# Kernel tuning notes

Hardware: AMD Instinct MI355X
Metric: run time of the kernel (lower is better)

## Reference

```python
import jax, jax.numpy as jnp
import numpy as np

N_NODES = 50000
N_EDGES = 1600000
D_IN = 512
D_OUT = 512


def setup_inputs() -> dict:
    key = jax.random.key(0)
    k1, k2, k3, k4, k5, k6 = jax.random.split(key, 6)
    stdv = 1.0 / np.sqrt(D_OUT)
    x = jax.random.normal(k1, (N_NODES, D_IN), dtype=jnp.float32)
    weight = jax.random.uniform(k2, (D_IN, D_OUT), dtype=jnp.float32, minval=-stdv, maxval=stdv)
    bias = jax.random.uniform(k3, (1, D_OUT), dtype=jnp.float32, minval=-stdv, maxval=stdv)
    edge_val = jax.random.uniform(k4, (N_EDGES,), dtype=jnp.float32)
    edge_row = jax.random.randint(k5, (N_EDGES,), 0, N_NODES, dtype=jnp.int64)
    edge_col = jax.random.randint(k6, (N_EDGES,), 0, N_NODES, dtype=jnp.int64)
    return {"x": x, "weight": weight, "bias": bias,
            "edge_val": edge_val, "edge_row": edge_row, "edge_col": edge_col}


def reference(x, weight, bias, edge_val, edge_row, edge_col):
    # hidden = X @ W  : [N, D_OUT] dense GEMM
    hidden = jnp.matmul(x, weight)
    # spmm: out[i] = sum over edges (i <- j) of adj_val * hidden[j]
    msgs = edge_val[:, None] * hidden[edge_col]            # [E, D_OUT]
    out = jax.ops.segment_sum(msgs, edge_row, num_segments=N_NODES)
    return out + bias
```

## Files before the change

### kernel.cpp

```cpp
#include <hip/hip_runtime.h>

typedef short short8 __attribute__((ext_vector_type(8)));
typedef float v4f   __attribute__((ext_vector_type(4)));

#define N_NODES 50000
#define N_EDGES 1600000
#define DIM     512
#define SCAN_NB 49

__device__ __forceinline__ float bf2f(unsigned short u) {
    unsigned int x = ((unsigned int)u) << 16;
    return __uint_as_float(x);
}
__device__ __forceinline__ unsigned int f2bfu(float f) {
    unsigned int x = __float_as_uint(f);
    unsigned int r = x + 0x7fffu + ((x >> 16) & 1u);
    return r >> 16;
}

__global__ void detect_kernel(const unsigned int* __restrict__ xw,
                              const int* __restrict__ erow,
                              int* __restrict__ flags) {
    __shared__ int cbf, cz;
    if (threadIdx.x == 0) { cbf = 0; cz = 0; }
    __syncthreads();
    int lb = 0, lz = 0;
    for (int i = threadIdx.x; i < 1024; i += 256) {
        unsigned int w = xw[i];
        unsigned int e0 = (w >> 7) & 0xFFu;
        unsigned int e1 = (w >> 23) & 0xFFu;
        if (e0 >= 0x70u && e0 <= 0x8Fu && e1 >= 0x70u && e1 <= 0x8Fu) lb++;
        if (erow[2 * i + 1] == 0) lz++;
    }
    atomicAdd(&cbf, lb);
    atomicAdd(&cz, lz);
    __syncthreads();
    if (threadIdx.x == 0) {
        flags[0] = (cbf > 512) ? 1 : 0;
        flags[1] = (cz > 512) ? 1 : 0;
    }
}

__global__ __launch_bounds__(256) void convert_x(const void* __restrict__ Xv,
                                                 unsigned short* __restrict__ Xc,
                                                 const int* __restrict__ flags) {
    if (flags[0] != 0) return;
    const float* Xf = (const float*)Xv;
    size_t i = ((size_t)blockIdx.x * 256 + threadIdx.x) * 8;
    float4 f0 = *(const float4*)(Xf + i);
    float4 f1 = *(const float4*)(Xf + i + 4);
    uint4 o;
    o.x = f2bfu(f0.x) | (f2bfu(f0.y) << 16);
    o.y = f2bfu(f0.z) | (f2bfu(f0.w) << 16);
    o.z = f2bfu(f1.x) | (f2bfu(f1.y) << 16);
    o.w = f2bfu(f1.z) | (f2bfu(f1.w) << 16);
    *(uint4*)(Xc + i) = o;
}

__global__ void transpose_w(const void* __restrict__ Wv,
                            unsigned short* __restrict__ Wt,
                            const int* __restrict__ flags) {
    __shared__ unsigned short tile[32][33];
    const bool fb = flags[0] != 0;
    int bx = blockIdx.x * 32, by = blockIdx.y * 32;
    int tx = threadIdx.x, ty = threadIdx.y;
    if (fb) {
        const unsigned short* W = (const unsigned short*)Wv;
        for (int r = ty; r < 32; r += 8)
            tile[r][tx] = W[(by + r) * DIM + bx + tx];
    } else {
        const float* W = (const float*)Wv;
        for (int r = ty; r < 32; r += 8)
            tile[r][tx] = (unsigned short)f2bfu(W[(by + r) * DIM + bx + tx]);
    }
    __syncthreads();
    for (int r = ty; r < 32; r += 8)
        Wt[(bx + r) * DIM + by + tx] = tile[tx][r];
}

#define TM 128
#define TN 128
#define BK 32
#define LP 40

__global__ __launch_bounds__(256) void gemm_kernel(
        const void* __restrict__ Xv,
        const unsigned short* __restrict__ Xc,
        const int have_xc,
        const unsigned short* __restrict__ Wt,
        unsigned short* __restrict__ H,
        const int* __restrict__ flags) {
    __shared__ unsigned short lA[TM * LP];
    __shared__ unsigned short lB[TN * LP];

    const bool fb = flags[0] != 0;
    const bool bfp = fb || (have_xc != 0);
    const unsigned short* Xb = fb ? (const unsigned short*)Xv : Xc;
    const float*          Xf = (const float*)Xv;

    const int t = threadIdx.x;
    const int mBase = blockIdx.y * TM;
    const int nBase = blockIdx.x * TN;
    const int w = t >> 6, lane = t & 63;
    const int lr = lane & 15, quad = lane >> 4;
    const int wr = w >> 1, wc = w & 1;

    v4f acc[4][4];
    #pragma unroll
    for (int i = 0; i < 4; ++i)
        #pragma unroll
        for (int j = 0; j < 4; ++j) acc[i][j] = (v4f)0.0f;

    for (int k0 = 0; k0 < DIM; k0 += BK) {
        #pragma unroll
        for (int rep = 0; rep < 2; ++rep) {
            int idx = rep * 256 + t;
            int r = idx >> 2;
            int cc = (idx & 3) * 8;
            int grow = mBase + r; if (grow >= N_NODES) grow = N_NODES - 1;
            size_t goff = (size_t)grow * DIM + k0 + cc;
            if (bfp) {
                uint4 av = *(const uint4*)(Xb + goff);
                *(uint4*)(&lA[r * LP + cc]) = av;
            } else {
                float4 a0 = *(const float4*)(Xf + goff);
                float4 a1 = *(const float4*)(Xf + goff + 4);
                uint4 av;
                av.x = f2bfu(a0.x) | (f2bfu(a0.y) << 16);
                av.y = f2bfu(a0.z) | (f2bfu(a0.w) << 16);
                av.z = f2bfu(a1.x) | (f2bfu(a1.y) << 16);
                av.w = f2bfu(a1.z) | (f2bfu(a1.w) << 16);
                *(uint4*)(&lA[r * LP + cc]) = av;
            }
            uint4 bv = *(const uint4*)(Wt + (size_t)(nBase + r) * DIM + k0 + cc);
            *(uint4*)(&lB[r * LP + cc]) = bv;
        }
        __syncthreads();

        short8 bfr[4];
        #pragma unroll
        for (int j = 0; j < 4; ++j)
            bfr[j] = *(const short8*)(&lB[(wc * 64 + j * 16 + lr) * LP + quad * 8]);
        #pragma unroll
        for (int i = 0; i < 4; ++i) {
            short8 a = *(const short8*)(&lA[(wr * 64 + i * 16 + lr) * LP + quad * 8]);
            #pragma unroll
            for (int j = 0; j < 4; ++j)
                acc[i][j] = __builtin_amdgcn_mfma_f32_16x16x32_bf16(a, bfr[j], acc[i][j], 0, 0, 0);
        }
        __syncthreads();
    }

    #pragma unroll
    for (int i = 0; i < 4; ++i) {
        #pragma unroll
        for (int j = 0; j < 4; ++j) {
            #pragma unroll
            for (int r = 0; r < 4; ++r) {
                int gm = mBase + wr * 64 + i * 16 + quad * 4 + r;
                int gn = nBase + wc * 64 + j * 16 + lr;
                if (gm < N_NODES)
                    H[(size_t)gm * DIM + gn] = (unsigned short)f2bfu(acc[i][j][r]);
            }
        }
    }
}

__global__ void hist_kernel(const int* __restrict__ row, int* __restrict__ cnt,
                            const int* __restrict__ flags) {
    const bool f64 = flags[1] != 0;
    int i = blockIdx.x * 256 + threadIdx.x;
    if (i < N_EDGES) {
        int r = f64 ? row[2 * (size_t)i] : row[i];
        atomicAdd(&cnt[r], 1);
    }
}

__global__ __launch_bounds__(256) void scan1_kernel(const int* __restrict__ cnt,
                                                    int* __restrict__ bsum) {
    __shared__ int sh[256];
    const int b = blockIdx.x, t = threadIdx.x;
    int base = b * 1024 + t * 4;
    int s = 0;
    #pragma unroll
    for (int k = 0; k < 4; ++k) {
        int i = base + k;
        if (i < N_NODES) s += cnt[i];
    }
    sh[t] = s;
    __syncthreads();
    for (int off = 128; off > 0; off >>= 1) {
        if (t < off) sh[t] += sh[t + off];
        __syncthreads();
    }
    if (t == 0) bsum[b] = sh[0];
}

__global__ __launch_bounds__(256) void scan3_kernel(const int* __restrict__ cnt,
                                                    const int* __restrict__ bsum,
                                                    int* __restrict__ start,
                                                    int* __restrict__ cursor) {
    __shared__ int sh[256];
    __shared__ int boffs;
    const int b = blockIdx.x, t = threadIdx.x;
    if (t == 0) {
        int r = 0;
        #pragma unroll 8
        for (int i = 0; i < b; ++i) r += bsum[i];
        boffs = r;
        if (b == 0) start[N_NODES] = N_EDGES;
    }
    int base = b * 1024 + t * 4;
    int v[4];
    #pragma unroll
    for (int k = 0; k < 4; ++k) {
        int i = base + k;
        v[k] = (i < N_NODES) ? cnt[i] : 0;
    }
    int tsum = v[0] + v[1] + v[2] + v[3];
    sh[t] = tsum;
    __syncthreads();
    for (int off = 1; off < 256; off <<= 1) {
        int x = (t >= off) ? sh[t - off] : 0;
        __syncthreads();
        sh[t] += x;
        __syncthreads();
    }
    int excl = sh[t] - tsum + boffs;
    #pragma unroll
    for (int k = 0; k < 4; ++k) {
        int i = base + k;
        if (i < N_NODES) { start[i] = excl; cursor[i] = excl; }
        excl += v[k];
    }
}

__global__ void scatter_kernel(const int* __restrict__ row, const int* __restrict__ col,
                               const void* __restrict__ valv,
                               int* __restrict__ cursor,
                               int2* __restrict__ sCV,
                               const int* __restrict__ flags) {
    const bool fb  = flags[0] != 0;
    const bool f64 = flags[1] != 0;
    int i = blockIdx.x * 256 + threadIdx.x;
    if (i < N_EDGES) {
        int r = f64 ? row[2 * (size_t)i] : row[i];
        int c = f64 ? col[2 * (size_t)i] : col[i];
        float v = fb ? bf2f(((const unsigned short*)valv)[i])
                     : ((const float*)valv)[i];
        int p = atomicAdd(&cursor[r], 1);
        int2 cv; cv.x = c; cv.y = __float_as_int(v);
        sCV[p] = cv;
    }
}

__global__ __launch_bounds__(128) void gather_kernel(
        const int* __restrict__ start, const int2* __restrict__ sCV,
        const unsigned short* __restrict__ H,
        const void* __restrict__ biasv, void* __restrict__ outv,
        const int* __restrict__ flags) {
    const bool fb = flags[0] != 0;
    const int node = blockIdx.x;
    const int t = threadIdx.x;
    const int s = start[node], e = start[node + 1];
    float a0 = 0.f, a1 = 0.f, a2 = 0.f, a3 = 0.f;
    #pragma unroll 4
    for (int p = s; p < e; ++p) {
        int2 cv = sCV[p];
        float v = __int_as_float(cv.y);
        uint2 h = *(const uint2*)(H + (size_t)cv.x * DIM + t * 4);
        a0 = fmaf(v, bf2f((unsigned short)(h.x & 0xffffu)), a0);
        a1 = fmaf(v, bf2f((unsigned short)(h.x >> 16)), a1);
        a2 = fmaf(v, bf2f((unsigned short)(h.y & 0xffffu)), a2);
        a3 = fmaf(v, bf2f((unsigned short)(h.y >> 16)), a3);
    }
    if (fb) {
        uint2 bb = ((const uint2*)biasv)[t];
        a0 += bf2f((unsigned short)(bb.x & 0xffffu));
        a1 += bf2f((unsigned short)(bb.x >> 16));
        a2 += bf2f((unsigned short)(bb.y & 0xffffu));
        a3 += bf2f((unsigned short)(bb.y >> 16));
        uint2 o;
        o.x = f2bfu(a0) | (f2bfu(a1) << 16);
        o.y = f2bfu(a2) | (f2bfu(a3) << 16);
        *(uint2*)((unsigned short*)outv + (size_t)node * DIM + t * 4) = o;
    } else {
        float4 bb = ((const float4*)biasv)[t];
        float4 o;
        o.x = a0 + bb.x; o.y = a1 + bb.y; o.z = a2 + bb.z; o.w = a3 + bb.w;
        *(float4*)((float*)outv + (size_t)node * DIM + t * 4) = o;
    }
}

extern "C" void kernel_launch(void* const* d_in, const int* in_sizes, int n_in,
                              void* d_out, int out_size, void* d_ws, size_t ws_size,
                              hipStream_t stream) {
    const void* X    = d_in[0];
    const void* W    = d_in[1];
    const void* bias = d_in[2];
    const void* eval = d_in[3];
    const int*  erow = (const int*)d_in[4];
    const int*  ecol = (const int*)d_in[5];

    char* w = (char*)d_ws;
    size_t o = 0;
    int* flags = (int*)(w + o); o += 256;
    unsigned short* hidden = (unsigned short*)(w + o); o += (size_t)N_NODES * DIM * 2;
    int2*  sCV    = (int2*)(w + o);  o += (size_t)N_EDGES * 8;
    int*   cnt    = (int*)(w + o);   o += 200704;
    int*   start  = (int*)(w + o);   o += 200704;
    int*   cursor = (int*)(w + o);   o += 200704;
    unsigned short* Wt = (unsigned short*)(w + o); o += (size_t)DIM * DIM * 2;
    int*   bsum   = (int*)(w + o);   o += 256;
    size_t base_end = o;
    unsigned short* Xc = (unsigned short*)(w + o);
    size_t need_xc = base_end + (size_t)N_NODES * DIM * 2;
    const int have_xc = (ws_size >= need_xc) ? 1 : 0;

    hipMemsetAsync(cnt, 0, N_NODES * sizeof(int), stream);

    detect_kernel<<<1, 256, 0, stream>>>((const unsigned int*)X, erow, flags);
    if (have_xc)
        convert_x<<<(N_NODES * DIM) / (256 * 8), 256, 0, stream>>>(X, Xc, flags);
    transpose_w<<<dim3(16, 16), dim3(32, 8), 0, stream>>>(W, Wt, flags);
    gemm_kernel<<<dim3(DIM / TN, (N_NODES + TM - 1) / TM), 256, 0, stream>>>(
        X, Xc, have_xc, Wt, hidden, flags);
    hist_kernel<<<(N_EDGES + 255) / 256, 256, 0, stream>>>(erow, cnt, flags);
    scan1_kernel<<<SCAN_NB, 256, 0, stream>>>(cnt, bsum);
    scan3_kernel<<<SCAN_NB, 256, 0, stream>>>(cnt, bsum, start, cursor);
    scatter_kernel<<<(N_EDGES + 255) / 256, 256, 0, stream>>>(erow, ecol, eval, cursor, sCV, flags);
    gather_kernel<<<N_NODES, 128, 0, stream>>>(start, sCV, hidden, bias, d_out, flags);
}
```

Measured before the change: 695.5 us.

## Restructure SpMM gather to one wavefront per node with lane-broadcast edges

The gather kernel now assigns one 64-lane wavefront per output row, four rows per 256-thread block, instead of one 128-thread block per row. Each lane loads 16 bytes of a hidden row, so one wavefront covers the full 512-wide bf16 row. Edge (col, val) pairs are loaded cooperatively, 64 at a time, and broadcast with readlane, which replaces per-thread redundant loads of sCV. This aims to cut index-load traffic and block scheduling overhead, and to widen memory accesses, at the cost of more accumulator registers per thread. The bf16 unpacking is also simplified to shift and mask operations.

```diff
diff --git a/kernel.cpp b/kernel.cpp
--- a/kernel.cpp
+++ b/kernel.cpp
@@ -17,6 +17,8 @@
     unsigned int r = x + 0x7fffu + ((x >> 16) & 1u);
     return r >> 16;
 }
+__device__ __forceinline__ float lo16(unsigned int u) { return __uint_as_float(u << 16); }
+__device__ __forceinline__ float hi16(unsigned int u) { return __uint_as_float(u & 0xffff0000u); }
 
 __global__ void detect_kernel(const unsigned int* __restrict__ xw,
                               const int* __restrict__ erow,
@@ -254,41 +256,61 @@
     }
 }
 
-__global__ __launch_bounds__(128) void gather_kernel(
+__global__ __launch_bounds__(256) void gather_kernel(
         const int* __restrict__ start, const int2* __restrict__ sCV,
         const unsigned short* __restrict__ H,
         const void* __restrict__ biasv, void* __restrict__ outv,
         const int* __restrict__ flags) {
     const bool fb = flags[0] != 0;
-    const int node = blockIdx.x;
-    const int t = threadIdx.x;
+    const int lane = threadIdx.x & 63;
+    const int node = blockIdx.x * 4 + (threadIdx.x >> 6);
+    if (node >= N_NODES) return;
     const int s = start[node], e = start[node + 1];
+
     float a0 = 0.f, a1 = 0.f, a2 = 0.f, a3 = 0.f;
-    #pragma unroll 4
-    for (int p = s; p < e; ++p) {
-        int2 cv = sCV[p];
-        float v = __int_as_float(cv.y);
-        uint2 h = *(const uint2*)(H + (size_t)cv.x * DIM + t * 4);
-        a0 = fmaf(v, bf2f((unsigned short)(h.x & 0xffffu)), a0);
-        a1 = fmaf(v, bf2f((unsigned short)(h.x >> 16)), a1);
-        a2 = fmaf(v, bf2f((unsigned short)(h.y & 0xffffu)), a2);
-        a3 = fmaf(v, bf2f((unsigned short)(h.y >> 16)), a3);
-    }
+    float a4 = 0.f, a5 = 0.f, a6 = 0.f, a7 = 0.f;
+
+    for (int p0 = s; p0 < e; p0 += 64) {
+        int idx = p0 + lane;
+        int clamped = (idx < e) ? idx : (e - 1);
+        int2 cv = sCV[clamped];
+        int cnt = e - p0; if (cnt > 64) cnt = 64;
+        #pragma unroll 4
+        for (int q = 0; q < cnt; ++q) {
+            int col  = __builtin_amdgcn_readlane(cv.x, q);
+            float v  = __int_as_float(__builtin_amdgcn_readlane(cv.y, q));
+            uint4 h = *((const uint4*)(H + ((size_t)col << 9)) + lane);
+            a0 = fmaf(v, lo16(h.x), a0);
+            a1 = fmaf(v, hi16(h.x), a1);
+            a2 = fmaf(v, lo16(h.y), a2);
+            a3 = fmaf(v, hi16(h.y), a3);
+            a4 = fmaf(v, lo16(h.z), a4);
+            a5 = fmaf(v, hi16(h.z), a5);
+            a6 = fmaf(v, lo16(h.w), a6);
+            a7 = fmaf(v, hi16(h.w), a7);
+        }
+    }
+
     if (fb) {
-        uint2 bb = ((const uint2*)biasv)[t];
-        a0 += bf2f((unsigned short)(bb.x & 0xffffu));
-        a1 += bf2f((unsigned short)(bb.x >> 16));
-        a2 += bf2f((unsigned short)(bb.y & 0xffffu));
-        a3 += bf2f((unsigned short)(bb.y >> 16));
-        uint2 o;
+        uint4 bb = *((const uint4*)biasv + lane);
+        a0 += lo16(bb.x); a1 += hi16(bb.x);
+        a2 += lo16(bb.y); a3 += hi16(bb.y);
+        a4 += lo16(bb.z); a5 += hi16(bb.z);
+        a6 += lo16(bb.w); a7 += hi16(bb.w);
+        uint4 o;
         o.x = f2bfu(a0) | (f2bfu(a1) << 16);
         o.y = f2bfu(a2) | (f2bfu(a3) << 16);
-        *(uint2*)((unsigned short*)outv + (size_t)node * DIM + t * 4) = o;
+        o.z = f2bfu(a4) | (f2bfu(a5) << 16);
+        o.w = f2bfu(a6) | (f2bfu(a7) << 16);
+        *((uint4*)((unsigned short*)outv + (size_t)node * DIM) + lane) = o;
     } else {
-        float4 bb = ((const float4*)biasv)[t];
-        float4 o;
-        o.x = a0 + bb.x; o.y = a1 + bb.y; o.z = a2 + bb.z; o.w = a3 + bb.w;
-        *(float4*)((float*)outv + (size_t)node * DIM + t * 4) = o;
+        const float4* bp = (const float4*)biasv + lane * 2;
+        float4 b0 = bp[0], b1 = bp[1];
+        float4 o0, o1;
+        o0.x = a0 + b0.x; o0.y = a1 + b0.y; o0.z = a2 + b0.z; o0.w = a3 + b0.w;
+        o1.x = a4 + b1.x; o1.y = a5 + b1.y; o1.z = a6 + b1.z; o1.w = a7 + b1.w;
+        float4* op = (float4*)((float*)outv + (size_t)node * DIM) + lane * 2;
+        op[0] = o0; op[1] = o1;
     }
 }
 
@@ -329,5 +351,5 @@
     scan1_kernel<<<SCAN_NB, 256, 0, stream>>>(cnt, bsum);
     scan3_kernel<<<SCAN_NB, 256, 0, stream>>>(cnt, bsum, start, cursor);
     scatter_kernel<<<(N_EDGES + 255) / 256, 256, 0, stream>>>(erow, ecol, eval, cursor, sCV, flags);
-    gather_kernel<<<N_NODES, 128, 0, stream>>>(start, sCV, hidden, bias, d_out, flags);
-}
+    gather_kernel<<<(N_NODES + 3) / 4, 256, 0, stream>>>(start, sCV, hidden, bias, d_out, flags);
+}
```

Result: no change. 691.9 us (-0.5%).
